# Optimization experiments

Hardware: AMD Instinct MI355X
Metric: run time of the kernel (lower is better)

The kernel has to match this reference:

```python
import math
import jax, jax.numpy as jnp
import numpy as np

K = 8
D = 8
LAMBDA_PRIOR = 0.01
TRI = D * (D + 1) // 2  # 36
PHI_DIM = K + K * D + K * TRI  # 360
_ROWS, _COLS = np.tril_indices(D)


def _unpack_phi(phi):
    # phi: [M, PHI_DIM] -> pi_tilde [M,K], mu [M,K,D], L_vecs [M,K,TRI]
    M = phi.shape[0]
    pi_tilde = phi[:, :K]
    mu = phi[:, K:K + K * D].reshape(M, K, D)
    L_vecs = phi[:, K + K * D:].reshape(M, K, TRI)
    return pi_tilde, mu, L_vecs


def _L_vec_to_matrix(L_vecs):
    # L_vecs: [M,K,TRI] -> lower-triangular L [M,K,D,D]
    M, Kc, _ = L_vecs.shape
    L = jnp.zeros((M, Kc, D, D), dtype=L_vecs.dtype)
    return L.at[:, :, _ROWS, _COLS].set(L_vecs)


def _gmm_log_likelihood(phi, X):
    # phi: [M, PHI_DIM], X: [N, D] -> log_lik [M]
    pi_tilde, mu, L_vecs = _unpack_phi(phi)
    log_pi = jax.nn.log_softmax(pi_tilde, axis=-1)          # [M,K]
    L = _L_vec_to_matrix(L_vecs)                             # [M,K,D,D]
    diff = X[None, None, :, :] - mu[:, :, None, :]           # [M,K,N,D]
    diff_T = jnp.swapaxes(diff, -1, -2)                      # [M,K,D,N]
    # solve L alpha = diff_T for each (m,k); batched triangular solve
    alpha = jax.scipy.linalg.solve_triangular(L, diff_T, lower=True)  # [M,K,D,N]
    maha = jnp.sum(alpha * alpha, axis=-2)                   # [M,K,N]
    log_diag = jnp.log(jnp.clip(jnp.abs(jnp.diagonal(L, axis1=-2, axis2=-1)), 1e-8))
    log_det = 2.0 * jnp.sum(log_diag, axis=-1)               # [M,K]
    log_norm_const = -0.5 * (D * math.log(2 * math.pi) + log_det[:, :, None])
    log_gauss = log_norm_const - 0.5 * maha                  # [M,K,N]
    log_mix = jax.scipy.special.logsumexp(log_pi[:, :, None] + log_gauss, axis=1)  # [M,N]
    return jnp.sum(log_mix, axis=-1)                         # [M]


def setup_inputs() -> dict:
    key = jax.random.key(0)
    k1, k2 = jax.random.split(key)
    M, N = 32, 32768
    phi = jax.random.normal(k1, (M, PHI_DIM), dtype=jnp.float32)
    X = jax.random.normal(k2, (N, D), dtype=jnp.float32)
    return {"phi": phi, "X": X}


def reference(phi, X):
    # U(phi; X) = -log p(X|phi) + lambda_prior * ||phi||^2 / 2  -> [M]
    log_lik = _gmm_log_likelihood(phi, X)
    prior = 0.5 * jnp.sum(phi * phi, axis=-1)
    return -log_lik + LAMBDA_PRIOR * prior
```

## Files before the change

kernel.cpp:

```cpp
#include <hip/hip_runtime.h>
#include <math.h>

#define KK 8
#define DD 8
#define TRI 36
#define PHI_DIM 360
#define MM 32
#define NN 32768
#define GX 16
#define TPB 256
#define PP 8
#define NPAIR 4

#define LOG2E 1.4426950408889634f
#define LN2   0.6931471805599453f
#define SSCALE 0.8493218002880191f
#define INV_SSCALE 1.177410022515475f

typedef float v2f __attribute__((ext_vector_type(2)));

__device__ __forceinline__ v2f splat(float s) { v2f r; r.x = s; r.y = s; return r; }

__launch_bounds__(TPB)
__global__ void gmm_kernel(const float* __restrict__ phi, const float* __restrict__ X,
                           float* __restrict__ out) {
    __shared__ float s_par[KK][48];
    __shared__ float s_red[TPB / 64];

    const int m = blockIdx.y;
    const float* __restrict__ ph = phi + m * PHI_DIM;
    const int tid = threadIdx.x;

    if (tid < KK) {
        const int k = tid;
        #pragma unroll
        for (int i = 0; i < DD; i++) s_par[k][i] = ph[KK + k * DD + i];

        float Lrow[TRI];
        #pragma unroll
        for (int t = 0; t < TRI; t++) Lrow[t] = ph[KK + KK * DD + k * TRI + t];

        float logdet = 0.f;
        #pragma unroll
        for (int i = 0; i < DD; i++) {
            const int di = i * (i + 1) / 2 + i;
            logdet += 2.f * __logf(fmaxf(fabsf(Lrow[di]), 1e-8f));
        }
        #pragma unroll
        for (int i = 0; i < DD; i++) {
            const int di = i * (i + 1) / 2 + i;
            #pragma unroll
            for (int j = 0; j < i; j++) {
                const int t = i * (i + 1) / 2 + j;
                s_par[k][8 + t] = Lrow[t] * INV_SSCALE;
            }
            s_par[k][8 + di] = SSCALE / Lrow[di];
        }
        float mx = ph[0];
        #pragma unroll
        for (int i = 1; i < KK; i++) mx = fmaxf(mx, ph[i]);
        float se = 0.f;
        #pragma unroll
        for (int i = 0; i < KK; i++) se += __expf(ph[i] - mx);
        const float lse = mx + __logf(se);
        const float c_ln = (ph[k] - lse) - 0.5f * (8.f * 1.8378770664093453f + logdet);
        s_par[k][44] = c_ln * LOG2E;
    }

    float pr = 0.f;
    if (blockIdx.x == 0) {
        for (int j = tid; j < PHI_DIM; j += TPB) {
            float v = ph[j];
            pr = fmaf(v, v, pr);
        }
    }
    __syncthreads();

    const int n0 = blockIdx.x * (NN / GX) + tid;
    v2f x[NPAIR][DD];
    #pragma unroll
    for (int q = 0; q < NPAIR; q++) {
        const float4* xa = (const float4*)(X + (size_t)(n0 + (2 * q) * TPB) * DD);
        const float4* xb = (const float4*)(X + (size_t)(n0 + (2 * q + 1) * TPB) * DD);
        float4 a0 = xa[0], a1 = xa[1], b0 = xb[0], b1 = xb[1];
        x[q][0].x = a0.x; x[q][0].y = b0.x;
        x[q][1].x = a0.y; x[q][1].y = b0.y;
        x[q][2].x = a0.z; x[q][2].y = b0.z;
        x[q][3].x = a0.w; x[q][3].y = b0.w;
        x[q][4].x = a1.x; x[q][4].y = b1.x;
        x[q][5].x = a1.y; x[q][5].y = b1.y;
        x[q][6].x = a1.z; x[q][6].y = b1.z;
        x[q][7].x = a1.w; x[q][7].y = b1.w;
    }

    v2f vk[NPAIR][KK];
    #pragma unroll
    for (int k = 0; k < KK; k++) {
        float cf[45];
        #pragma unroll
        for (int t = 0; t < 45; t++) cf[t] = s_par[k][t];

        const v2f c2 = splat(cf[44]);
        #pragma unroll
        for (int q = 0; q < NPAIR; q++) {
            v2f a[DD];
            v2f vv = c2;
            #pragma unroll
            for (int i = 0; i < DD; i++) {
                v2f t = x[q][i] - splat(cf[i]);
                #pragma unroll
                for (int j = 0; j < i; j++)
                    t = __builtin_elementwise_fma(splat(cf[8 + i * (i + 1) / 2 + j]), -a[j], t);
                a[i] = t * splat(cf[8 + i * (i + 1) / 2 + i]);
                vv = __builtin_elementwise_fma(-a[i], a[i], vv);
            }
            vk[q][k] = vv;
        }
    }

    float acc2 = 0.f;
    #pragma unroll
    for (int q = 0; q < NPAIR; q++) {
        v2f mx = vk[q][0];
        #pragma unroll
        for (int i = 1; i < KK; i++) mx = __builtin_elementwise_max(mx, vk[q][i]);
        v2f s = splat(0.f);
        #pragma unroll
        for (int i = 0; i < KK; i++) {
            v2f d = vk[q][i] - mx;
            s.x += __builtin_exp2f(d.x);
            s.y += __builtin_exp2f(d.y);
        }
        acc2 += mx.x + __builtin_log2f(s.x);
        acc2 += mx.y + __builtin_log2f(s.y);
    }

    float contrib = fmaf(-LN2, acc2, 0.005f * pr);

    #pragma unroll
    for (int off = 32; off; off >>= 1) contrib += __shfl_down(contrib, off, 64);
    if ((tid & 63) == 0) s_red[tid >> 6] = contrib;
    __syncthreads();
    if (tid == 0) {
        float t = s_red[0] + s_red[1] + s_red[2] + s_red[3];
        atomicAdd(&out[m], t);
    }
}

extern "C" void kernel_launch(void* const* d_in, const int* in_sizes, int n_in,
                              void* d_out, int out_size, void* d_ws, size_t ws_size,
                              hipStream_t stream) {
    const float* phi = (const float*)d_in[0];
    const float* X   = (const float*)d_in[1];
    float* out = (float*)d_out;

    dim3 grid(GX, MM);
    gmm_kernel<<<grid, TPB, 0, stream>>>(phi, X, out);
}
```

Measured before the change: 70.23 us.

## Precompute inverse Cholesky in prep kernel and use matrix-vector Mahalanobis

Adds a separate prep kernel that inverts each lower-triangular factor in double precision, folds the mean into a bias term and the log-normaliser into a constant, and writes the coefficients to workspace. The main kernel then computes each Mahalanobis term as a triangular mat-vec with FMAs instead of a forward substitution with a dependent chain and per-block parameter setup. The grid grows to 64x32 blocks with 2 points per thread and reads coefficients directly from global memory. This trades a second launch and a serialised prep step for a shorter dependency chain and more parallelism.

```diff
diff --git a/kernel.cpp b/kernel.cpp
--- a/kernel.cpp
+++ b/kernel.cpp
@@ -7,144 +7,142 @@
 #define PHI_DIM 360
 #define MM 32
 #define NN 32768
-#define GX 16
 #define TPB 256
-#define PP 8
-#define NPAIR 4
+#define GX 64
+#define CSTRIDE 48
 
 #define LOG2E 1.4426950408889634f
 #define LN2   0.6931471805599453f
-#define SSCALE 0.8493218002880191f
-#define INV_SSCALE 1.177410022515475f
 
 typedef float v2f __attribute__((ext_vector_type(2)));
+__device__ __forceinline__ v2f splat(float s) { v2f r; r.x = s; r.y = s; return r; }
+#define TIX(i, j) ((i) * ((i) + 1) / 2 + (j))
 
-__device__ __forceinline__ v2f splat(float s) { v2f r; r.x = s; r.y = s; return r; }
+__launch_bounds__(256)
+__global__ void prep_kernel(const float* __restrict__ phi,
+                            float* __restrict__ coef,
+                            float* __restrict__ out) {
+    const int t = threadIdx.x;
+    const int m = t >> 3, k = t & 7;
+    const float* __restrict__ ph = phi + m * PHI_DIM;
 
-__launch_bounds__(TPB)
-__global__ void gmm_kernel(const float* __restrict__ phi, const float* __restrict__ X,
-                           float* __restrict__ out) {
-    __shared__ float s_par[KK][48];
-    __shared__ float s_red[TPB / 64];
+    double mxp = (double)ph[0];
+    #pragma unroll
+    for (int i = 1; i < KK; i++) mxp = fmax(mxp, (double)ph[i]);
+    double se = 0.0;
+    #pragma unroll
+    for (int i = 0; i < KK; i++) se += exp((double)ph[i] - mxp);
+    const double lse = mxp + log(se);
 
-    const int m = blockIdx.y;
-    const float* __restrict__ ph = phi + m * PHI_DIM;
-    const int tid = threadIdx.x;
+    double Lr[TRI];
+    #pragma unroll
+    for (int j = 0; j < TRI; j++) Lr[j] = (double)ph[KK + KK * DD + k * TRI + j];
+    double mu[DD];
+    #pragma unroll
+    for (int i = 0; i < DD; i++) mu[i] = (double)ph[KK + k * DD + i];
 
-    if (tid < KK) {
-        const int k = tid;
+    double logdet = 0.0;
+    #pragma unroll
+    for (int i = 0; i < DD; i++)
+        logdet += 2.0 * log(fmax(fabs(Lr[TIX(i, i)]), 1e-8));
+
+    double B[TRI];
+    #pragma unroll
+    for (int i = 0; i < DD; i++) {
+        const double inv = 1.0 / Lr[TIX(i, i)];
+        B[TIX(i, i)] = inv;
         #pragma unroll
-        for (int i = 0; i < DD; i++) s_par[k][i] = ph[KK + k * DD + i];
-
-        float Lrow[TRI];
-        #pragma unroll
-        for (int t = 0; t < TRI; t++) Lrow[t] = ph[KK + KK * DD + k * TRI + t];
-
-        float logdet = 0.f;
-        #pragma unroll
-        for (int i = 0; i < DD; i++) {
-            const int di = i * (i + 1) / 2 + i;
-            logdet += 2.f * __logf(fmaxf(fabsf(Lrow[di]), 1e-8f));
-        }
-        #pragma unroll
-        for (int i = 0; i < DD; i++) {
-            const int di = i * (i + 1) / 2 + i;
+        for (int j = 0; j < i; j++) {
+            double s = 0.0;
             #pragma unroll
-            for (int j = 0; j < i; j++) {
-                const int t = i * (i + 1) / 2 + j;
-                s_par[k][8 + t] = Lrow[t] * INV_SSCALE;
-            }
-            s_par[k][8 + di] = SSCALE / Lrow[di];
-        }
-        float mx = ph[0];
-        #pragma unroll
-        for (int i = 1; i < KK; i++) mx = fmaxf(mx, ph[i]);
-        float se = 0.f;
-        #pragma unroll
-        for (int i = 0; i < KK; i++) se += __expf(ph[i] - mx);
-        const float lse = mx + __logf(se);
-        const float c_ln = (ph[k] - lse) - 0.5f * (8.f * 1.8378770664093453f + logdet);
-        s_par[k][44] = c_ln * LOG2E;
-    }
-
-    float pr = 0.f;
-    if (blockIdx.x == 0) {
-        for (int j = tid; j < PHI_DIM; j += TPB) {
-            float v = ph[j];
-            pr = fmaf(v, v, pr);
-        }
-    }
-    __syncthreads();
-
-    const int n0 = blockIdx.x * (NN / GX) + tid;
-    v2f x[NPAIR][DD];
-    #pragma unroll
-    for (int q = 0; q < NPAIR; q++) {
-        const float4* xa = (const float4*)(X + (size_t)(n0 + (2 * q) * TPB) * DD);
-        const float4* xb = (const float4*)(X + (size_t)(n0 + (2 * q + 1) * TPB) * DD);
-        float4 a0 = xa[0], a1 = xa[1], b0 = xb[0], b1 = xb[1];
-        x[q][0].x = a0.x; x[q][0].y = b0.x;
-        x[q][1].x = a0.y; x[q][1].y = b0.y;
-        x[q][2].x = a0.z; x[q][2].y = b0.z;
-        x[q][3].x = a0.w; x[q][3].y = b0.w;
-        x[q][4].x = a1.x; x[q][4].y = b1.x;
-        x[q][5].x = a1.y; x[q][5].y = b1.y;
-        x[q][6].x = a1.z; x[q][6].y = b1.z;
-        x[q][7].x = a1.w; x[q][7].y = b1.w;
-    }
-
-    v2f vk[NPAIR][KK];
-    #pragma unroll
-    for (int k = 0; k < KK; k++) {
-        float cf[45];
-        #pragma unroll
-        for (int t = 0; t < 45; t++) cf[t] = s_par[k][t];
-
-        const v2f c2 = splat(cf[44]);
-        #pragma unroll
-        for (int q = 0; q < NPAIR; q++) {
-            v2f a[DD];
-            v2f vv = c2;
-            #pragma unroll
-            for (int i = 0; i < DD; i++) {
-                v2f t = x[q][i] - splat(cf[i]);
-                #pragma unroll
-                for (int j = 0; j < i; j++)
-                    t = __builtin_elementwise_fma(splat(cf[8 + i * (i + 1) / 2 + j]), -a[j], t);
-                a[i] = t * splat(cf[8 + i * (i + 1) / 2 + i]);
-                vv = __builtin_elementwise_fma(-a[i], a[i], vv);
-            }
-            vk[q][k] = vv;
+            for (int p = j; p < i; p++) s += Lr[TIX(i, p)] * B[TIX(p, j)];
+            B[TIX(i, j)] = -inv * s;
         }
     }
 
-    float acc2 = 0.f;
+    const double SS = 0.84932180028801904272;
+    float* __restrict__ ck = coef + (size_t)(m * KK + k) * CSTRIDE;
     #pragma unroll
-    for (int q = 0; q < NPAIR; q++) {
-        v2f mx = vk[q][0];
+    for (int r = 0; r < TRI; r++) ck[r] = (float)(SS * B[r]);
+    #pragma unroll
+    for (int i = 0; i < DD; i++) {
+        double nd = 0.0;
         #pragma unroll
-        for (int i = 1; i < KK; i++) mx = __builtin_elementwise_max(mx, vk[q][i]);
-        v2f s = splat(0.f);
+        for (int j = 0; j <= i; j++) nd += B[TIX(i, j)] * mu[j];
+        ck[TRI + i] = (float)(-SS * nd);
+    }
+    const double c2 = (((double)ph[k] - lse)
+                       - 0.5 * (8.0 * 1.8378770664093454836 + logdet))
+                      * 1.4426950408889634074;
+    ck[44] = (float)c2;
+
+    float pr = 0.f;
+    #pragma unroll
+    for (int j = 0; j < 45; j++) {
+        const float v = ph[k * 45 + j];
+        pr = fmaf(v, v, pr);
+    }
+    pr += __shfl_down(pr, 4, 8);
+    pr += __shfl_down(pr, 2, 8);
+    pr += __shfl_down(pr, 1, 8);
+    if (k == 0) atomicAdd(&out[m], 0.005f * pr);
+}
+
+__launch_bounds__(TPB, 4)
+__global__ void gmm_main(const float* __restrict__ X,
+                         const float* __restrict__ coef,
+                         float* __restrict__ out) {
+    __shared__ float s_red[TPB / 64];
+    const int m = blockIdx.y;
+    const int tid = threadIdx.x;
+    const int n0 = blockIdx.x * (2 * TPB) + tid;
+
+    const float4* xa = (const float4*)(X + (size_t)n0 * DD);
+    const float4* xb = (const float4*)(X + (size_t)(n0 + TPB) * DD);
+    const float4 a0 = xa[0], a1 = xa[1], b0 = xb[0], b1 = xb[1];
+    v2f x[DD];
+    x[0].x = a0.x; x[0].y = b0.x;  x[1].x = a0.y; x[1].y = b0.y;
+    x[2].x = a0.z; x[2].y = b0.z;  x[3].x = a0.w; x[3].y = b0.w;
+    x[4].x = a1.x; x[4].y = b1.x;  x[5].x = a1.y; x[5].y = b1.y;
+    x[6].x = a1.z; x[6].y = b1.z;  x[7].x = a1.w; x[7].y = b1.w;
+
+    const float* __restrict__ cb = coef + (size_t)m * (KK * CSTRIDE);
+    v2f vk[KK];
+    #pragma unroll
+    for (int k = 0; k < KK; k++) {
+        const float* __restrict__ ck = cb + k * CSTRIDE;
+        v2f vv = splat(ck[44]);
         #pragma unroll
-        for (int i = 0; i < KK; i++) {
-            v2f d = vk[q][i] - mx;
-            s.x += __builtin_exp2f(d.x);
-            s.y += __builtin_exp2f(d.y);
+        for (int i = 0; i < DD; i++) {
+            const int r = TIX(i, 0);
+            v2f t = __builtin_elementwise_fma(splat(ck[r]), x[0], splat(ck[TRI + i]));
+            #pragma unroll
+            for (int j = 1; j <= i; j++)
+                t = __builtin_elementwise_fma(splat(ck[r + j]), x[j], t);
+            vv = __builtin_elementwise_fma(-t, t, vv);
         }
-        acc2 += mx.x + __builtin_log2f(s.x);
-        acc2 += mx.y + __builtin_log2f(s.y);
+        vk[k] = vv;
     }
 
-    float contrib = fmaf(-LN2, acc2, 0.005f * pr);
+    v2f mx = vk[0];
+    #pragma unroll
+    for (int i = 1; i < KK; i++) mx = __builtin_elementwise_max(mx, vk[i]);
+    v2f s = splat(0.f);
+    #pragma unroll
+    for (int i = 0; i < KK; i++) {
+        const v2f d = vk[i] - mx;
+        s.x += __builtin_exp2f(d.x);
+        s.y += __builtin_exp2f(d.y);
+    }
+    const float acc2 = mx.x + __builtin_log2f(s.x) + mx.y + __builtin_log2f(s.y);
+    float contrib = -LN2 * acc2;
 
     #pragma unroll
     for (int off = 32; off; off >>= 1) contrib += __shfl_down(contrib, off, 64);
     if ((tid & 63) == 0) s_red[tid >> 6] = contrib;
     __syncthreads();
-    if (tid == 0) {
-        float t = s_red[0] + s_red[1] + s_red[2] + s_red[3];
-        atomicAdd(&out[m], t);
-    }
+    if (tid == 0)
+        atomicAdd(&out[m], s_red[0] + s_red[1] + s_red[2] + s_red[3]);
 }
 
 extern "C" void kernel_launch(void* const* d_in, const int* in_sizes, int n_in,
@@ -152,8 +150,9 @@
                               hipStream_t stream) {
     const float* phi = (const float*)d_in[0];
     const float* X   = (const float*)d_in[1];
-    float* out = (float*)d_out;
+    float* out  = (float*)d_out;
+    float* coef = (float*)d_ws;
 
-    dim3 grid(GX, MM);
-    gmm_kernel<<<grid, TPB, 0, stream>>>(phi, X, out);
+    prep_kernel<<<dim3(1), 256, 0, stream>>>(phi, coef, out);
+    gmm_main<<<dim3(GX, MM), TPB, 0, stream>>>(X, coef, out);
 }
```

Measured after the change: 85.79 us. +22.2%, slower.

## Precompute inverse Cholesky factor so per-point solve becomes independent dot products

Applied to the files above, without the earlier changes.

The setup threads now invert each lower-triangular L in double precision and fold the mean into a per-row offset (-L^{-1} mu). The per-point forward substitution, a serial dependency chain, becomes independent FMA dot products. The grid is also doubled in x while points per thread are halved, and launch bounds request 4 blocks per SM to raise occupancy. The risk is that the setup threads now do costlier double-precision math, and coefficients are read from shared memory inside the inner loop rather than cached in registers.

```diff
diff --git a/kernel.cpp b/kernel.cpp
--- a/kernel.cpp
+++ b/kernel.cpp
@@ -7,21 +7,18 @@
 #define PHI_DIM 360
 #define MM 32
 #define NN 32768
-#define GX 16
 #define TPB 256
-#define PP 8
-#define NPAIR 4
+#define GX 32
+#define NPAIR 2
 
 #define LOG2E 1.4426950408889634f
 #define LN2   0.6931471805599453f
-#define SSCALE 0.8493218002880191f
-#define INV_SSCALE 1.177410022515475f
 
 typedef float v2f __attribute__((ext_vector_type(2)));
+__device__ __forceinline__ v2f splat(float s) { v2f r; r.x = s; r.y = s; return r; }
+#define TIX(i, j) ((i) * ((i) + 1) / 2 + (j))
 
-__device__ __forceinline__ v2f splat(float s) { v2f r; r.x = s; r.y = s; return r; }
-
-__launch_bounds__(TPB)
+__launch_bounds__(TPB, 4)
 __global__ void gmm_kernel(const float* __restrict__ phi, const float* __restrict__ X,
                            float* __restrict__ out) {
     __shared__ float s_par[KK][48];
@@ -33,38 +30,54 @@
 
     if (tid < KK) {
         const int k = tid;
+        float Lr[TRI];
         #pragma unroll
-        for (int i = 0; i < DD; i++) s_par[k][i] = ph[KK + k * DD + i];
+        for (int t = 0; t < TRI; t++) Lr[t] = ph[KK + KK * DD + k * TRI + t];
+        float muv[DD];
+        #pragma unroll
+        for (int i = 0; i < DD; i++) muv[i] = ph[KK + k * DD + i];
 
-        float Lrow[TRI];
+        double logdet = 0.0;
         #pragma unroll
-        for (int t = 0; t < TRI; t++) Lrow[t] = ph[KK + KK * DD + k * TRI + t];
+        for (int i = 0; i < DD; i++)
+            logdet += 2.0 * log(fmax(fabs((double)Lr[TIX(i, i)]), 1e-8));
 
-        float logdet = 0.f;
+        double mxp = (double)ph[0];
         #pragma unroll
-        for (int i = 0; i < DD; i++) {
-            const int di = i * (i + 1) / 2 + i;
-            logdet += 2.f * __logf(fmaxf(fabsf(Lrow[di]), 1e-8f));
+        for (int i = 1; i < KK; i++) mxp = fmax(mxp, (double)ph[i]);
+        double se = 0.0;
+        #pragma unroll
+        for (int i = 0; i < KK; i++) se += exp((double)ph[i] - mxp);
+        const double lse = mxp + log(se);
+
+        const double SS = 0.84932180028801904272;
+        double nd[DD];
+        #pragma unroll
+        for (int i = 0; i < DD; i++) nd[i] = 0.0;
+        #pragma unroll
+        for (int j = 0; j < DD; j++) {
+            double col[DD];
+            col[j] = 1.0 / (double)Lr[TIX(j, j)];
+            #pragma unroll
+            for (int i = j + 1; i < DD; i++) {
+                double s = 0.0;
+                #pragma unroll
+                for (int p = j; p < i; p++) s += (double)Lr[TIX(i, p)] * col[p];
+                col[i] = -s / (double)Lr[TIX(i, i)];
+            }
+            #pragma unroll
+            for (int i = j; i < DD; i++) {
+                s_par[k][8 + TIX(i, j)] = (float)(SS * col[i]);
+                nd[i] += col[i] * (double)muv[j];
+            }
         }
         #pragma unroll
-        for (int i = 0; i < DD; i++) {
-            const int di = i * (i + 1) / 2 + i;
-            #pragma unroll
-            for (int j = 0; j < i; j++) {
-                const int t = i * (i + 1) / 2 + j;
-                s_par[k][8 + t] = Lrow[t] * INV_SSCALE;
-            }
-            s_par[k][8 + di] = SSCALE / Lrow[di];
-        }
-        float mx = ph[0];
-        #pragma unroll
-        for (int i = 1; i < KK; i++) mx = fmaxf(mx, ph[i]);
-        float se = 0.f;
-        #pragma unroll
-        for (int i = 0; i < KK; i++) se += __expf(ph[i] - mx);
-        const float lse = mx + __logf(se);
-        const float c_ln = (ph[k] - lse) - 0.5f * (8.f * 1.8378770664093453f + logdet);
-        s_par[k][44] = c_ln * LOG2E;
+        for (int i = 0; i < DD; i++) s_par[k][i] = (float)(-SS * nd[i]);
+
+        const double c2 = (((double)ph[k] - lse)
+                           - 0.5 * (8.0 * 1.8378770664093454836 + logdet))
+                          * 1.4426950408889634074;
+        s_par[k][44] = (float)c2;
     }
 
     float pr = 0.f;
@@ -96,26 +109,26 @@
     v2f vk[NPAIR][KK];
     #pragma unroll
     for (int k = 0; k < KK; k++) {
-        float cf[45];
+        v2f vv0 = splat(s_par[k][44]);
+        v2f vv1 = vv0;
         #pragma unroll
-        for (int t = 0; t < 45; t++) cf[t] = s_par[k][t];
-
-        const v2f c2 = splat(cf[44]);
-        #pragma unroll
-        for (int q = 0; q < NPAIR; q++) {
-            v2f a[DD];
-            v2f vv = c2;
+        for (int i = 0; i < DD; i++) {
+            const int r = 8 + TIX(i, 0);
+            const float ndi = s_par[k][i];
+            const float a0 = s_par[k][r];
+            v2f t0 = __builtin_elementwise_fma(splat(a0), x[0][0], splat(ndi));
+            v2f t1 = __builtin_elementwise_fma(splat(a0), x[1][0], splat(ndi));
             #pragma unroll
-            for (int i = 0; i < DD; i++) {
-                v2f t = x[q][i] - splat(cf[i]);
-                #pragma unroll
-                for (int j = 0; j < i; j++)
-                    t = __builtin_elementwise_fma(splat(cf[8 + i * (i + 1) / 2 + j]), -a[j], t);
-                a[i] = t * splat(cf[8 + i * (i + 1) / 2 + i]);
-                vv = __builtin_elementwise_fma(-a[i], a[i], vv);
+            for (int j = 1; j <= i; j++) {
+                const float aj = s_par[k][r + j];
+                t0 = __builtin_elementwise_fma(splat(aj), x[0][j], t0);
+                t1 = __builtin_elementwise_fma(splat(aj), x[1][j], t1);
             }
-            vk[q][k] = vv;
+            vv0 = __builtin_elementwise_fma(-t0, t0, vv0);
+            vv1 = __builtin_elementwise_fma(-t1, t1, vv1);
         }
+        vk[0][k] = vv0;
+        vk[1][k] = vv1;
     }
 
     float acc2 = 0.f;
```

Result: slower. 73.96 us (+5.3%).
